# Kernel optimization log

Measured on AMD Instinct MI355X. Metric: run time of the kernel, lower is better.

The kernel has to match this reference:

```python
import jax, jax.numpy as jnp
import numpy as np

N, E, B = 50000, 800000, 128
H, L, FIN, GF = 256, 4, 8, 85
LN_EPS = 1e-5


def _ln(x, g, b):
    m = jnp.mean(x, axis=-1, keepdims=True)
    v = jnp.var(x, axis=-1, keepdims=True)
    return g * (x - m) * jax.lax.rsqrt(v + LN_EPS) + b


def setup_inputs() -> dict:
    key = jax.random.key(0)
    ks = iter(jax.random.split(key, 40))

    def nrm(shape, scale):
        return jax.random.normal(next(ks), shape, jnp.float32) * scale

    inp = {}
    inp["x"] = nrm((N, FIN), 1.0)
    inp["edge_index"] = jax.random.randint(next(ks), (2, E), 0, N, dtype=jnp.int32)
    inp["edge_weight"] = jax.random.uniform(next(ks), (E,), jnp.float32)
    inp["batch"] = jnp.sort(jax.random.randint(next(ks), (N,), 0, B, dtype=jnp.int32))
    inp["gene_feat"] = nrm((B, GF), 1.0)
    # input projection
    inp["W_in"] = nrm((FIN, H), FIN ** -0.5); inp["b_in"] = jnp.zeros((H,), jnp.float32)
    inp["ln_in_g"] = jnp.ones((H,), jnp.float32); inp["ln_in_b"] = jnp.zeros((H,), jnp.float32)
    # GIN layers (stacked over L)
    inp["eps"] = jnp.zeros((L,), jnp.float32)
    inp["W1"] = nrm((L, H, 2 * H), H ** -0.5); inp["b1"] = jnp.zeros((L, 2 * H), jnp.float32)
    inp["W2"] = nrm((L, 2 * H, H), (2 * H) ** -0.5); inp["b2"] = jnp.zeros((L, H), jnp.float32)
    inp["ln_g"] = jnp.ones((L, H), jnp.float32); inp["ln_b"] = jnp.zeros((L, H), jnp.float32)
    # gene feature projection
    inp["Wg1"] = nrm((GF, H), GF ** -0.5); inp["bg1"] = jnp.zeros((H,), jnp.float32)
    inp["lng_g"] = jnp.ones((H,), jnp.float32); inp["lng_b"] = jnp.zeros((H,), jnp.float32)
    inp["Wg2"] = nrm((H, H // 2), H ** -0.5); inp["bg2"] = jnp.zeros((H // 2,), jnp.float32)
    # classifier (embed_dim = 2H + H//2 = 640)
    ED = 2 * H + H // 2
    inp["Wc1"] = nrm((ED, H), ED ** -0.5); inp["bc1"] = jnp.zeros((H,), jnp.float32)
    inp["Wc2"] = nrm((H, H // 2), H ** -0.5); inp["bc2"] = jnp.zeros((H // 2,), jnp.float32)
    inp["Wc3"] = nrm((H // 2, 2), (H // 2) ** -0.5); inp["bc3"] = jnp.zeros((2,), jnp.float32)
    return inp


def reference(x, edge_index, edge_weight, batch, gene_feat,
              W_in, b_in, ln_in_g, ln_in_b,
              eps, W1, b1, W2, b2, ln_g, ln_b,
              Wg1, bg1, lng_g, lng_b, Wg2, bg2,
              Wc1, bc1, Wc2, bc2, Wc3, bc3):
    n = x.shape[0]
    nb = gene_feat.shape[0]
    # input projection: Linear -> LayerNorm -> ReLU  (dropout = eval mode)
    h = jax.nn.relu(_ln(x @ W_in + b_in, ln_in_g, ln_in_b))
    src, dst = edge_index[0], edge_index[1]
    for i in range(W1.shape[0]):
        res = h
        # weighted GIN aggregation; self-loops with weight 1 fold into (2+eps)*h
        msg = h[src] * edge_weight[:, None]            # [E, H]
        agg = jax.ops.segment_sum(msg, dst, num_segments=n)
        out = (2.0 + eps[i]) * h + agg
        out = jax.nn.relu(out @ W1[i] + b1[i]) @ W2[i] + b2[i]
        h = jax.nn.relu(_ln(out, ln_g[i], ln_b[i])) + res
    # dual pooling (mean + max) per graph
    counts = jax.ops.segment_sum(jnp.ones((n,), h.dtype), batch, num_segments=nb)
    gmean = jax.ops.segment_sum(h, batch, num_segments=nb) / jnp.clip(counts, 1.0)[:, None]
    gmax = jax.ops.segment_max(h, batch, num_segments=nb)
    gmax = jnp.where(jnp.isfinite(gmax), gmax, 0.0)
    # gene feature projection
    gp = jax.nn.relu(_ln(gene_feat @ Wg1 + bg1, lng_g, lng_b))
    gp = jax.nn.relu(gp @ Wg2 + bg2)
    g = jnp.concatenate([gmean, gmax, gp], axis=-1)   # [B, 640]
    # classifier
    hc = jax.nn.relu(g @ Wc1 + bc1)
    hc = jax.nn.relu(hc @ Wc2 + bc2)
    return hc @ Wc3 + bc3
```

## Files before the change

### kernel.cpp

```cpp
#include <hip/hip_runtime.h>
#include <hip/hip_bf16.h>

#define N_NODES 50000
#define MP 50048
#define N_EDGES 800000
#define N_B 128
#define H_DIM 256
#define H2_DIM 512
#define FIN_DIM 8
#define GF_DIM 85
#define LN_EPS 1e-5f
#define SCAN_NBLK 196

typedef unsigned short u16;
typedef unsigned int u32;
typedef _Float16 f16;
typedef __attribute__((ext_vector_type(8))) _Float16 f16x8;
typedef __attribute__((ext_vector_type(8))) unsigned short u16x8;
typedef __attribute__((ext_vector_type(4))) float f32x4;

__device__ inline float relu_f(float x) { return x > 0.f ? x : 0.f; }

__device__ inline float h2f(u16 b) { f16 h; __builtin_memcpy(&h, &b, 2); return (float)h; }
__device__ inline u16 f2h(float x) { f16 h = (f16)x; u16 b; __builtin_memcpy(&b, &h, 2); return b; }

#define GLOAD16(gp, lp) __builtin_amdgcn_global_load_lds( \
    (const __attribute__((address_space(1))) void*)(gp),  \
    (__attribute__((address_space(3))) void*)(lp), 16, 0, 0)

__device__ inline void ln_stats_256(float v, float* sbuf, float& mean, float& rstd) {
    float s = v, s2 = v * v;
#pragma unroll
    for (int off = 32; off > 0; off >>= 1) {
        s += __shfl_down(s, off);
        s2 += __shfl_down(s2, off);
    }
    int t = threadIdx.x;
    if ((t & 63) == 0) { sbuf[t >> 6] = s; sbuf[4 + (t >> 6)] = s2; }
    __syncthreads();
    float ts = sbuf[0] + sbuf[1] + sbuf[2] + sbuf[3];
    float ts2 = sbuf[4] + sbuf[5] + sbuf[6] + sbuf[7];
    mean = ts * (1.f / H_DIM);
    float var = ts2 * (1.f / H_DIM) - mean * mean;
    rstd = rsqrtf(var + LN_EPS);
}

__global__ void k_input_proj(const float* __restrict__ x, const float* __restrict__ Wi,
                             const float* __restrict__ bi, const float* __restrict__ g,
                             const float* __restrict__ bb,
                             u16* __restrict__ Hh, u16* __restrict__ Hl) {
    int n = blockIdx.x, t = threadIdx.x;
    __shared__ float xs[FIN_DIM];
    __shared__ float sbuf[8];
    if (t < FIN_DIM) xs[t] = x[n * FIN_DIM + t];
    __syncthreads();
    float acc = bi[t];
#pragma unroll
    for (int k = 0; k < FIN_DIM; ++k) acc = fmaf(xs[k], Wi[k * H_DIM + t], acc);
    float mean, rstd;
    ln_stats_256(acc, sbuf, mean, rstd);
    float v = relu_f(g[t] * (acc - mean) * rstd + bb[t]);
    u16 hh = f2h(v);
    size_t o = (size_t)n * H_DIM + t;
    Hh[o] = hh;
    Hl[o] = f2h(v - h2f(hh));
}

__global__ void k_hist(const int* __restrict__ ei, int* __restrict__ deg) {
    int e = blockIdx.x * 256 + threadIdx.x;
    atomicAdd(&deg[ei[N_EDGES + e]], 1);
}

__global__ void k_scan1(const int* __restrict__ deg, int* __restrict__ row_start,
                        int* __restrict__ bsum) {
    __shared__ int s[256];
    int t = threadIdx.x, i = blockIdx.x * 256 + t;
    int v = (i < N_NODES) ? deg[i] : 0;
    s[t] = v;
    __syncthreads();
    for (int off = 1; off < 256; off <<= 1) {
        int x = (t >= off) ? s[t - off] : 0;
        __syncthreads();
        s[t] += x;
        __syncthreads();
    }
    if (i < N_NODES) row_start[i] = s[t] - v;
    if (t == 255) bsum[blockIdx.x] = s[255];
}

__global__ void k_scan2(int* __restrict__ bsum) {
    __shared__ int s[256];
    int t = threadIdx.x;
    int v = (t < SCAN_NBLK) ? bsum[t] : 0;
    s[t] = v;
    __syncthreads();
    for (int off = 1; off < 256; off <<= 1) {
        int x = (t >= off) ? s[t - off] : 0;
        __syncthreads();
        s[t] += x;
        __syncthreads();
    }
    if (t < SCAN_NBLK) bsum[t] = s[t] - v;
}

__global__ void k_scan3(int* __restrict__ row_start, const int* __restrict__ bsum) {
    int t = threadIdx.x, i = blockIdx.x * 256 + t;
    if (i < N_NODES) row_start[i] += bsum[blockIdx.x];
    if (i == 0) row_start[N_NODES] = N_EDGES;
}

__global__ void k_scatter(const int* __restrict__ ei, const float* __restrict__ ew,
                          const int* __restrict__ row_start, int* __restrict__ cursor,
                          int* __restrict__ csr_src, float* __restrict__ csr_w) {
    int e = blockIdx.x * 256 + threadIdx.x;
    int d = ei[N_EDGES + e];
    int p = atomicAdd(&cursor[d], 1);
    int i = row_start[d] + p;
    csr_src[i] = ei[e];
    csr_w[i] = ew[e];
}

__global__ void k_gbounds(const int* __restrict__ batch, int* __restrict__ gstart,
                          int* __restrict__ gcnt) {
    __shared__ int s[N_B + 1];
    int b = threadIdx.x;
    int lo = 0, hi = N_NODES;
    while (lo < hi) {
        int mid = (lo + hi) >> 1;
        if (batch[mid] < b) lo = mid + 1; else hi = mid;
    }
    s[b] = lo;
    if (b == 0) s[N_B] = N_NODES;
    __syncthreads();
    gstart[b] = s[b];
    gcnt[b] = s[b + 1] - s[b];
}

__global__ void k_agg(const u16* __restrict__ Hh, const u16* __restrict__ Hl,
                      const int* __restrict__ row_start,
                      const int* __restrict__ csr_src, const float* __restrict__ csr_w,
                      const float* __restrict__ eps, int layer,
                      u16* __restrict__ Ah) {
    const int n = blockIdx.x, t = threadIdx.x, wv = t >> 6, lane = t & 63;
    const int half = lane >> 5, sl = lane & 31;
    __shared__ int s_src[256];
    __shared__ float s_w[256];
    __shared__ float part[4][256];
    int start = row_start[n], end = row_start[n + 1];
    float a[8];
#pragma unroll
    for (int q = 0; q < 8; ++q) a[q] = 0.f;
    for (int e0 = start; e0 < end; e0 += 256) {
        int ne = end - e0; if (ne > 256) ne = 256;
        if (t < ne) { s_src[t] = csr_src[e0 + t]; s_w[t] = csr_w[e0 + t]; }
        __syncthreads();
        for (int j = wv * 2 + half; j < ne; j += 8) {
            int src = s_src[j];
            float w = s_w[j];
            u16x8 v = *reinterpret_cast<const u16x8*>(&Hh[(size_t)src * H_DIM + sl * 8]);
#pragma unroll
            for (int q = 0; q < 8; ++q) a[q] = fmaf(w, h2f(v[q]), a[q]);
        }
        __syncthreads();
    }
#pragma unroll
    for (int q = 0; q < 8; ++q) a[q] += __shfl_xor(a[q], 32);
    if (half == 0) {
        *reinterpret_cast<float4*>(&part[wv][sl * 8]) = (float4){a[0], a[1], a[2], a[3]};
        *reinterpret_cast<float4*>(&part[wv][sl * 8 + 4]) = (float4){a[4], a[5], a[6], a[7]};
    }
    __syncthreads();
    float sum = part[0][t] + part[1][t] + part[2][t] + part[3][t];
    size_t so = (size_t)n * H_DIM + t;
    float e2 = 2.0f + eps[layer];
    float hs = h2f(Hh[so]) + h2f(Hl[so]);
    Ah[so] = f2h(e2 * hs + sum);
}

__global__ void k_wprep(const float* __restrict__ W, u16* __restrict__ T, int R, int C) {
    __shared__ float tile[64][65];
    int c0 = blockIdx.x * 64, r0 = blockIdx.y * 64;
    const float* Wl = W + (size_t)blockIdx.z * R * C;
    u16* Tl_ = T + (size_t)blockIdx.z * R * C;
    int t = threadIdx.x;
    int col = t & 63, qr = t >> 6;
#pragma unroll
    for (int i = 0; i < 16; ++i) {
        int row = i * 4 + qr;
        tile[row][col] = Wl[(size_t)(r0 + row) * C + c0 + col];
    }
    __syncthreads();
#pragma unroll
    for (int i = 0; i < 16; ++i) {
        int crow = i * 4 + qr;
        Tl_[(size_t)(c0 + crow) * R + r0 + col] = f2h(tile[col][crow]);
    }
}

__global__ __launch_bounds__(256, 2) void k_mgemm1(
    const u16* __restrict__ Ah, const u16* __restrict__ Wt,
    const float* __restrict__ bias, u16* __restrict__ Ch) {
    __shared__ __align__(16) u16 sA[128 * 32];
    __shared__ __align__(16) u16 sB[128 * 32];
    const int t = threadIdx.x;
    const int wv = t >> 6, lane = t & 63;
    const int fr = lane & 15, kg = lane >> 4;
    const int m0 = blockIdx.x * 128, n0 = blockIdx.y * 128;
    const int wm = (wv >> 1) * 64, wn = (wv & 1) * 64;

    f32x4 acc[4][4];
#pragma unroll
    for (int i = 0; i < 4; ++i)
#pragma unroll
        for (int j = 0; j < 4; ++j) acc[i][j] = (f32x4){0.f, 0.f, 0.f, 0.f};

    for (int k0 = 0; k0 < 256; k0 += 32) {
#pragma unroll
        for (int is = 0; is < 2; ++is) {
            int chunk = wv * 128 + is * 64 + lane;
            int r = chunk >> 2, p = chunk & 3;
            int ps = p ^ ((r >> 1) & 3);
            size_t ea = (size_t)(m0 + r) * 256 + k0 + ps * 8;
            size_t eb = (size_t)(n0 + r) * 256 + k0 + ps * 8;
            int lbase = (wv * 128 + is * 64) * 8;
            GLOAD16(Ah + ea, &sA[lbase]);
            GLOAD16(Wt + eb, &sB[lbase]);
        }
        __syncthreads();
        f16x8 fa[4], fb[4];
#pragma unroll
        for (int mf = 0; mf < 4; ++mf) {
            int row = wm + mf * 16 + fr;
            fa[mf] = *(const f16x8*)&sA[row * 32 + ((kg ^ ((row >> 1) & 3)) << 3)];
        }
#pragma unroll
        for (int nf = 0; nf < 4; ++nf) {
            int row = wn + nf * 16 + fr;
            fb[nf] = *(const f16x8*)&sB[row * 32 + ((kg ^ ((row >> 1) & 3)) << 3)];
        }
#pragma unroll
        for (int mf = 0; mf < 4; ++mf)
#pragma unroll
            for (int nf = 0; nf < 4; ++nf)
                acc[mf][nf] = __builtin_amdgcn_mfma_f32_16x16x32_f16(fa[mf], fb[nf], acc[mf][nf], 0, 0, 0);
        __syncthreads();
    }
#pragma unroll
    for (int nf = 0; nf < 4; ++nf) {
        int col = n0 + wn + nf * 16 + fr;
        float bi = bias[col];
#pragma unroll
        for (int mf = 0; mf < 4; ++mf)
#pragma unroll
            for (int j = 0; j < 4; ++j) {
                int grow = m0 + wm + mf * 16 + kg * 4 + j;
                Ch[(size_t)grow * 512 + col] = f2h(relu_f(acc[mf][nf][j] + bi));
            }
    }
}

__global__ __launch_bounds__(256, 2) void k_mgemm2(
    const u16* __restrict__ Ah, const u16* __restrict__ Wt,
    const float* __restrict__ bias, const float* __restrict__ lg,
    const float* __restrict__ lbv,
    const u16* __restrict__ Rh, const u16* __restrict__ Rl,
    u16* __restrict__ Oh, u16* __restrict__ Ol) {
    __shared__ __align__(16) u16 sA[64 * 32];
    __shared__ __align__(16) u16 sB[256 * 32];
    __shared__ float lnS[64][4], lnS2[64][4];
    __shared__ float lnm[64], lnr[64];
    const int t = threadIdx.x;
    const int wv = t >> 6, lane = t & 63;
    const int fr = lane & 15, kg = lane >> 4;
    const int m0 = blockIdx.x * 64;

    f32x4 acc[4][4];
#pragma unroll
    for (int i = 0; i < 4; ++i)
#pragma unroll
        for (int j = 0; j < 4; ++j) acc[i][j] = (f32x4){0.f, 0.f, 0.f, 0.f};

    for (int k0 = 0; k0 < 512; k0 += 32) {
        {
            int r = t >> 2, p = t & 3;
            int ps = p ^ ((r >> 1) & 3);
            size_t ea = (size_t)(m0 + r) * 512 + k0 + ps * 8;
            int lbase = (wv * 64) * 8;
            GLOAD16(Ah + ea, &sA[lbase]);
        }
#pragma unroll
        for (int is = 0; is < 4; ++is) {
            int chunk = is * 256 + t;
            int r = chunk >> 2, p = chunk & 3;
            int ps = p ^ ((r >> 1) & 3);
            size_t eb = (size_t)r * 512 + k0 + ps * 8;
            int lbase = (is * 256 + wv * 64) * 8;
            GLOAD16(Wt + eb, &sB[lbase]);
        }
        __syncthreads();
        f16x8 fa[4], fb[4];
#pragma unroll
        for (int mf = 0; mf < 4; ++mf) {
            int row = mf * 16 + fr;
            fa[mf] = *(const f16x8*)&sA[row * 32 + ((kg ^ ((row >> 1) & 3)) << 3)];
        }
#pragma unroll
        for (int nf = 0; nf < 4; ++nf) {
            int row = wv * 64 + nf * 16 + fr;
            fb[nf] = *(const f16x8*)&sB[row * 32 + ((kg ^ ((row >> 1) & 3)) << 3)];
        }
#pragma unroll
        for (int mf = 0; mf < 4; ++mf)
#pragma unroll
            for (int nf = 0; nf < 4; ++nf)
                acc[mf][nf] = __builtin_amdgcn_mfma_f32_16x16x32_f16(fa[mf], fb[nf], acc[mf][nf], 0, 0, 0);
        __syncthreads();
    }
    float bcol[4];
#pragma unroll
    for (int nf = 0; nf < 4; ++nf) bcol[nf] = bias[wv * 64 + nf * 16 + fr];
#pragma unroll
    for (int mf = 0; mf < 4; ++mf)
#pragma unroll
        for (int nf = 0; nf < 4; ++nf)
#pragma unroll
            for (int j = 0; j < 4; ++j) acc[mf][nf][j] += bcol[nf];
#pragma unroll
    for (int mf = 0; mf < 4; ++mf)
#pragma unroll
        for (int j = 0; j < 4; ++j) {
            float s = acc[mf][0][j] + acc[mf][1][j] + acc[mf][2][j] + acc[mf][3][j];
            float s2 = acc[mf][0][j] * acc[mf][0][j] + acc[mf][1][j] * acc[mf][1][j] +
                       acc[mf][2][j] * acc[mf][2][j] + acc[mf][3][j] * acc[mf][3][j];
#pragma unroll
            for (int off = 1; off < 16; off <<= 1) {
                s += __shfl_xor(s, off);
                s2 += __shfl_xor(s2, off);
            }
            if (fr == 0) {
                int row = mf * 16 + kg * 4 + j;
                lnS[row][wv] = s;
                lnS2[row][wv] = s2;
            }
        }
    __syncthreads();
    if (t < 64) {
        float s = lnS[t][0] + lnS[t][1] + lnS[t][2] + lnS[t][3];
        float s2 = lnS2[t][0] + lnS2[t][1] + lnS2[t][2] + lnS2[t][3];
        float m = s * (1.f / 256.f);
        float var = s2 * (1.f / 256.f) - m * m;
        lnm[t] = m;
        lnr[t] = rsqrtf(var + LN_EPS);
    }
    __syncthreads();
    float gg[4], bb[4];
#pragma unroll
    for (int nf = 0; nf < 4; ++nf) {
        int col = wv * 64 + nf * 16 + fr;
        gg[nf] = lg[col];
        bb[nf] = lbv[col];
    }
#pragma unroll
    for (int mf = 0; mf < 4; ++mf)
#pragma unroll
        for (int j = 0; j < 4; ++j) {
            int row = mf * 16 + kg * 4 + j;
            int grow = m0 + row;
            float m = lnm[row], rs = lnr[row];
#pragma unroll
            for (int nf = 0; nf < 4; ++nf) {
                int col = wv * 64 + nf * 16 + fr;
                size_t o = (size_t)grow * 256 + col;
                float res = h2f(Rh[o]) + h2f(Rl[o]);
                float v = relu_f(gg[nf] * (acc[mf][nf][j] - m) * rs + bb[nf]) + res;
                u16 hh = f2h(v);
                Oh[o] = hh;
                Ol[o] = f2h(v - h2f(hh));
            }
        }
}

__global__ void k_pool(const u16* __restrict__ Hh, const u16* __restrict__ Hl,
                       const int* __restrict__ gstart,
                       const int* __restrict__ gcnt, float* __restrict__ g) {
    int b = blockIdx.x;
    int col = blockIdx.y * 64 + (threadIdx.x & 63);
    int r = threadIdx.x >> 6;
    int st = gstart[b], cnt = gcnt[b];
    float s = 0.f, mx = -3.4e38f;
    for (int i = r; i < cnt; i += 4) {
        size_t o = (size_t)(st + i) * H_DIM + col;
        float v = h2f(Hh[o]) + h2f(Hl[o]);
        s += v;
        mx = fmaxf(mx, v);
    }
    __shared__ float ss[256], sm[256];
    ss[threadIdx.x] = s;
    sm[threadIdx.x] = mx;
    __syncthreads();
    if (r == 0) {
#pragma unroll
        for (int k = 1; k < 4; ++k) {
            s += ss[threadIdx.x + 64 * k];
            mx = fmaxf(mx, sm[threadIdx.x + 64 * k]);
        }
        float mean = cnt > 0 ? s / (float)cnt : 0.f;
        if (cnt == 0) mx = 0.f;
        g[b * 640 + col] = mean;
        g[b * 640 + 256 + col] = mx;
    }
}

__global__ void k_gene(const float* __restrict__ gf, const float* __restrict__ Wg1,
                       const float* __restrict__ bg1, const float* __restrict__ lg,
                       const float* __restrict__ lb, const float* __restrict__ Wg2,
                       const float* __restrict__ bg2, float* __restrict__ g) {
    int b = blockIdx.x, t = threadIdx.x;
    __shared__ float xs[GF_DIM];
    __shared__ float sbuf[8];
    __shared__ float s1[H_DIM];
    if (t < GF_DIM) xs[t] = gf[b * GF_DIM + t];
    __syncthreads();
    float acc = bg1[t];
    for (int k = 0; k < GF_DIM; ++k) acc = fmaf(xs[k], Wg1[k * H_DIM + t], acc);
    float mean, rstd;
    ln_stats_256(acc, sbuf, mean, rstd);
    s1[t] = relu_f(lg[t] * (acc - mean) * rstd + lb[t]);
    __syncthreads();
    if (t < 128) {
        float a2 = bg2[t];
        for (int k = 0; k < H_DIM; ++k) a2 = fmaf(s1[k], Wg2[k * 128 + t], a2);
        g[b * 640 + 512 + t] = relu_f(a2);
    }
}

__global__ void k_cls(const float* __restrict__ g, const float* __restrict__ Wc1,
                      const float* __restrict__ bc1, const float* __restrict__ Wc2,
                      const float* __restrict__ bc2, const float* __restrict__ Wc3,
                      const float* __restrict__ bc3, float* __restrict__ out) {
    int b = blockIdx.x, t = threadIdx.x;
    __shared__ float gg[640];
    __shared__ float s1[256];
    __shared__ float s2[128];
    gg[t] = g[b * 640 + t];
    gg[t + 256] = g[b * 640 + 256 + t];
    if (t < 128) gg[t + 512] = g[b * 640 + 512 + t];
    __syncthreads();
    float a = bc1[t];
    for (int k = 0; k < 640; ++k) a = fmaf(gg[k], Wc1[k * 256 + t], a);
    s1[t] = relu_f(a);
    __syncthreads();
    if (t < 128) {
        float a2 = bc2[t];
        for (int k = 0; k < 256; ++k) a2 = fmaf(s1[k], Wc2[k * 128 + t], a2);
        s2[t] = relu_f(a2);
    }
    __syncthreads();
    if (t < 2) {
        float a3 = bc3[t];
        for (int k = 0; k < 128; ++k) a3 = fmaf(s2[k], Wc3[k * 2 + t], a3);
        out[b * 2 + t] = a3;
    }
}

extern "C" void kernel_launch(void* const* d_in, const int* in_sizes, int n_in,
                              void* d_out, int out_size, void* d_ws, size_t ws_size,
                              hipStream_t stream) {
    const float* x = (const float*)d_in[0];
    const int* ei = (const int*)d_in[1];
    const float* ew = (const float*)d_in[2];
    const int* batch = (const int*)d_in[3];
    const float* gf = (const float*)d_in[4];
    const float* W_in = (const float*)d_in[5];
    const float* b_in = (const float*)d_in[6];
    const float* ln_in_g = (const float*)d_in[7];
    const float* ln_in_b = (const float*)d_in[8];
    const float* eps = (const float*)d_in[9];
    const float* W1 = (const float*)d_in[10];
    const float* b1 = (const float*)d_in[11];
    const float* W2 = (const float*)d_in[12];
    const float* b2 = (const float*)d_in[13];
    const float* ln_g = (const float*)d_in[14];
    const float* ln_b = (const float*)d_in[15];
    const float* Wg1 = (const float*)d_in[16];
    const float* bg1 = (const float*)d_in[17];
    const float* lng_g = (const float*)d_in[18];
    const float* lng_b = (const float*)d_in[19];
    const float* Wg2 = (const float*)d_in[20];
    const float* bg2 = (const float*)d_in[21];
    const float* Wc1 = (const float*)d_in[22];
    const float* bc1 = (const float*)d_in[23];
    const float* Wc2 = (const float*)d_in[24];
    const float* bc2 = (const float*)d_in[25];
    const float* Wc3 = (const float*)d_in[26];
    const float* bc3 = (const float*)d_in[27];
    float* out = (float*)d_out;

    char* ws = (char*)d_ws;
    size_t off = 0;
    auto alloc = [&](size_t bytes) -> char* {
        char* p = ws + off;
        off += (bytes + 255) & ~(size_t)255;
        return p;
    };
    u16* Hh0 = (u16*)alloc((size_t)MP * H_DIM * 2);
    u16* Hl0 = (u16*)alloc((size_t)MP * H_DIM * 2);
    u16* Hh1 = (u16*)alloc((size_t)MP * H_DIM * 2);
    u16* Hl1 = (u16*)alloc((size_t)MP * H_DIM * 2);
    u16* Ah = (u16*)alloc((size_t)MP * H_DIM * 2);
    u16* C1h = (u16*)alloc((size_t)MP * H2_DIM * 2);
    u16* W1T = (u16*)alloc((size_t)4 * H2_DIM * H_DIM * 2);
    u16* W2T = (u16*)alloc((size_t)4 * H_DIM * H2_DIM * 2);
    int* deg = (int*)alloc(N_NODES * 4);
    int* cursor = (int*)alloc(N_NODES * 4);
    int* row_start = (int*)alloc((N_NODES + 1) * 4);
    int* bsum = (int*)alloc(256 * 4);
    int* gcnt = (int*)alloc(N_B * 4);
    int* gstart = (int*)alloc(N_B * 4);
    int* csr_src = (int*)alloc(N_EDGES * 4);
    float* csr_w = (float*)alloc(N_EDGES * 4);
    float* gbuf = (float*)alloc(N_B * 640 * 4);
    (void)ws_size; (void)in_sizes; (void)n_in; (void)out_size;

    hipMemsetAsync(deg, 0, (size_t)((char*)row_start - (char*)deg), stream);

    k_wprep<<<dim3(H2_DIM / 64, H_DIM / 64, 4), 256, 0, stream>>>(W1, W1T, H_DIM, H2_DIM);
    k_wprep<<<dim3(H_DIM / 64, H2_DIM / 64, 4), 256, 0, stream>>>(W2, W2T, H2_DIM, H_DIM);

    k_input_proj<<<N_NODES, 256, 0, stream>>>(x, W_in, b_in, ln_in_g, ln_in_b, Hh0, Hl0);
    k_hist<<<N_EDGES / 256, 256, 0, stream>>>(ei, deg);
    k_scan1<<<SCAN_NBLK, 256, 0, stream>>>(deg, row_start, bsum);
    k_scan2<<<1, 256, 0, stream>>>(bsum);
    k_scan3<<<SCAN_NBLK, 256, 0, stream>>>(row_start, bsum);
    k_scatter<<<N_EDGES / 256, 256, 0, stream>>>(ei, ew, row_start, cursor, csr_src, csr_w);
    k_gbounds<<<1, N_B, 0, stream>>>(batch, gstart, gcnt);

    u16* hch = Hh0; u16* hcl = Hl0;
    u16* hnh = Hh1; u16* hnl = Hl1;
    for (int l = 0; l < 4; ++l) {
        k_agg<<<N_NODES, 256, 0, stream>>>(hch, hcl, row_start, csr_src, csr_w, eps, l, Ah);
        k_mgemm1<<<dim3(MP / 128, 4), 256, 0, stream>>>(
            Ah, W1T + (size_t)l * H2_DIM * H_DIM,
            b1 + (size_t)l * H2_DIM, C1h);
        k_mgemm2<<<MP / 64, 256, 0, stream>>>(
            C1h, W2T + (size_t)l * H_DIM * H2_DIM,
            b2 + (size_t)l * H_DIM, ln_g + (size_t)l * H_DIM, ln_b + (size_t)l * H_DIM,
            hch, hcl, hnh, hnl);
        u16* th = hch; hch = hnh; hnh = th;
        u16* tl = hcl; hcl = hnl; hnl = tl;
    }

    k_pool<<<dim3(N_B, 4), 256, 0, stream>>>(hch, hcl, gstart, gcnt, gbuf);
    k_gene<<<N_B, 256, 0, stream>>>(gf, Wg1, bg1, lng_g, lng_b, Wg2, bg2, gbuf);
    k_cls<<<N_B, 256, 0, stream>>>(gbuf, Wc1, bc1, Wc2, bc2, Wc3, bc3, out);
}
```

Before: 815.8 us.

## Use one 32-lane group per node in aggregation and widen GEMM K-tiles

The aggregation kernel now gives each node to a 32-lane group, with eight nodes per block, instead of one 256-thread block per node. Neighbor loads are unrolled by four, and the shared-memory staging, barriers and cross-wave reduction are removed. Both MFMA GEMMs now stage K tiles of 64 instead of 32 with a wider XOR swizzle, halving the number of barrier-separated K iterations. This trades more LDS per block and more registers, which could lower occupancy, for fewer syncs and more memory-level parallelism in the gather.

```diff
diff --git a/kernel.cpp b/kernel.cpp
--- a/kernel.cpp
+++ b/kernel.cpp
@@ -141,40 +141,45 @@
                       const int* __restrict__ csr_src, const float* __restrict__ csr_w,
                       const float* __restrict__ eps, int layer,
                       u16* __restrict__ Ah) {
-    const int n = blockIdx.x, t = threadIdx.x, wv = t >> 6, lane = t & 63;
-    const int half = lane >> 5, sl = lane & 31;
-    __shared__ int s_src[256];
-    __shared__ float s_w[256];
-    __shared__ float part[4][256];
+    const int t = threadIdx.x;
+    const int n = blockIdx.x * 8 + (t >> 5);
+    const int sl = t & 31;
     int start = row_start[n], end = row_start[n + 1];
     float a[8];
 #pragma unroll
     for (int q = 0; q < 8; ++q) a[q] = 0.f;
-    for (int e0 = start; e0 < end; e0 += 256) {
-        int ne = end - e0; if (ne > 256) ne = 256;
-        if (t < ne) { s_src[t] = csr_src[e0 + t]; s_w[t] = csr_w[e0 + t]; }
-        __syncthreads();
-        for (int j = wv * 2 + half; j < ne; j += 8) {
-            int src = s_src[j];
-            float w = s_w[j];
-            u16x8 v = *reinterpret_cast<const u16x8*>(&Hh[(size_t)src * H_DIM + sl * 8]);
-#pragma unroll
-            for (int q = 0; q < 8; ++q) a[q] = fmaf(w, h2f(v[q]), a[q]);
-        }
-        __syncthreads();
-    }
-#pragma unroll
-    for (int q = 0; q < 8; ++q) a[q] += __shfl_xor(a[q], 32);
-    if (half == 0) {
-        *reinterpret_cast<float4*>(&part[wv][sl * 8]) = (float4){a[0], a[1], a[2], a[3]};
-        *reinterpret_cast<float4*>(&part[wv][sl * 8 + 4]) = (float4){a[4], a[5], a[6], a[7]};
-    }
-    __syncthreads();
-    float sum = part[0][t] + part[1][t] + part[2][t] + part[3][t];
-    size_t so = (size_t)n * H_DIM + t;
+    int e = start;
+    for (; e + 3 < end; e += 4) {
+        int s0 = csr_src[e], s1 = csr_src[e + 1], s2 = csr_src[e + 2], s3 = csr_src[e + 3];
+        float w0 = csr_w[e], w1 = csr_w[e + 1], w2 = csr_w[e + 2], w3 = csr_w[e + 3];
+        u16x8 v0 = *reinterpret_cast<const u16x8*>(&Hh[(size_t)s0 * H_DIM + sl * 8]);
+        u16x8 v1 = *reinterpret_cast<const u16x8*>(&Hh[(size_t)s1 * H_DIM + sl * 8]);
+        u16x8 v2 = *reinterpret_cast<const u16x8*>(&Hh[(size_t)s2 * H_DIM + sl * 8]);
+        u16x8 v3 = *reinterpret_cast<const u16x8*>(&Hh[(size_t)s3 * H_DIM + sl * 8]);
+#pragma unroll
+        for (int q = 0; q < 8; ++q) {
+            a[q] = fmaf(w0, h2f(v0[q]), a[q]);
+            a[q] = fmaf(w1, h2f(v1[q]), a[q]);
+            a[q] = fmaf(w2, h2f(v2[q]), a[q]);
+            a[q] = fmaf(w3, h2f(v3[q]), a[q]);
+        }
+    }
+    for (; e < end; ++e) {
+        int src = csr_src[e];
+        float w = csr_w[e];
+        u16x8 v = *reinterpret_cast<const u16x8*>(&Hh[(size_t)src * H_DIM + sl * 8]);
+#pragma unroll
+        for (int q = 0; q < 8; ++q) a[q] = fmaf(w, h2f(v[q]), a[q]);
+    }
+    size_t so = (size_t)n * H_DIM + sl * 8;
     float e2 = 2.0f + eps[layer];
-    float hs = h2f(Hh[so]) + h2f(Hl[so]);
-    Ah[so] = f2h(e2 * hs + sum);
+    u16x8 hh = *reinterpret_cast<const u16x8*>(&Hh[so]);
+    u16x8 hl = *reinterpret_cast<const u16x8*>(&Hl[so]);
+    u16x8 o;
+#pragma unroll
+    for (int q = 0; q < 8; ++q)
+        o[q] = f2h(e2 * (h2f(hh[q]) + h2f(hl[q])) + a[q]);
+    *reinterpret_cast<u16x8*>(&Ah[so]) = o;
 }
 
 __global__ void k_wprep(const float* __restrict__ W, u16* __restrict__ T, int R, int C) {
@@ -200,8 +205,8 @@
 __global__ __launch_bounds__(256, 2) void k_mgemm1(
     const u16* __restrict__ Ah, const u16* __restrict__ Wt,
     const float* __restrict__ bias, u16* __restrict__ Ch) {
-    __shared__ __align__(16) u16 sA[128 * 32];
-    __shared__ __align__(16) u16 sB[128 * 32];
+    __shared__ __align__(16) u16 sA[128 * 64];
+    __shared__ __align__(16) u16 sB[128 * 64];
     const int t = threadIdx.x;
     const int wv = t >> 6, lane = t & 63;
     const int fr = lane & 15, kg = lane >> 4;
@@ -214,35 +219,43 @@
 #pragma unroll
         for (int j = 0; j < 4; ++j) acc[i][j] = (f32x4){0.f, 0.f, 0.f, 0.f};
 
-    for (int k0 = 0; k0 < 256; k0 += 32) {
-#pragma unroll
-        for (int is = 0; is < 2; ++is) {
-            int chunk = wv * 128 + is * 64 + lane;
-            int r = chunk >> 2, p = chunk & 3;
-            int ps = p ^ ((r >> 1) & 3);
-            size_t ea = (size_t)(m0 + r) * 256 + k0 + ps * 8;
-            size_t eb = (size_t)(n0 + r) * 256 + k0 + ps * 8;
-            int lbase = (wv * 128 + is * 64) * 8;
-            GLOAD16(Ah + ea, &sA[lbase]);
-            GLOAD16(Wt + eb, &sB[lbase]);
-        }
-        __syncthreads();
-        f16x8 fa[4], fb[4];
+    for (int k0 = 0; k0 < 256; k0 += 64) {
+#pragma unroll
+        for (int i = 0; i < 4; ++i) {
+            int ch = i * 256 + t;
+            int r = ch >> 3, p = ch & 7;
+            int ps = p ^ (r & 7);
+            int lbase = (i * 256 + wv * 64) * 8;
+            GLOAD16(Ah + (size_t)(m0 + r) * 256 + k0 + ps * 8, &sA[lbase]);
+            GLOAD16(Wt + (size_t)(n0 + r) * 256 + k0 + ps * 8, &sB[lbase]);
+        }
+        __syncthreads();
+        f16x8 fa[4][2], fb[4][2];
 #pragma unroll
         for (int mf = 0; mf < 4; ++mf) {
             int row = wm + mf * 16 + fr;
-            fa[mf] = *(const f16x8*)&sA[row * 32 + ((kg ^ ((row >> 1) & 3)) << 3)];
+#pragma unroll
+            for (int kk = 0; kk < 2; ++kk) {
+                int qs = (kk * 4 + kg) ^ (row & 7);
+                fa[mf][kk] = *(const f16x8*)&sA[row * 64 + qs * 8];
+            }
         }
 #pragma unroll
         for (int nf = 0; nf < 4; ++nf) {
             int row = wn + nf * 16 + fr;
-            fb[nf] = *(const f16x8*)&sB[row * 32 + ((kg ^ ((row >> 1) & 3)) << 3)];
-        }
-#pragma unroll
-        for (int mf = 0; mf < 4; ++mf)
-#pragma unroll
-            for (int nf = 0; nf < 4; ++nf)
-                acc[mf][nf] = __builtin_amdgcn_mfma_f32_16x16x32_f16(fa[mf], fb[nf], acc[mf][nf], 0, 0, 0);
+#pragma unroll
+            for (int kk = 0; kk < 2; ++kk) {
+                int qs = (kk * 4 + kg) ^ (row & 7);
+                fb[nf][kk] = *(const f16x8*)&sB[row * 64 + qs * 8];
+            }
+        }
+#pragma unroll
+        for (int kk = 0; kk < 2; ++kk)
+#pragma unroll
+            for (int mf = 0; mf < 4; ++mf)
+#pragma unroll
+                for (int nf = 0; nf < 4; ++nf)
+                    acc[mf][nf] = __builtin_amdgcn_mfma_f32_16x16x32_f16(fa[mf][kk], fb[nf][kk], acc[mf][nf], 0, 0, 0);
         __syncthreads();
     }
 #pragma unroll
@@ -265,8 +278,8 @@
     const float* __restrict__ lbv,
     const u16* __restrict__ Rh, const u16* __restrict__ Rl,
     u16* __restrict__ Oh, u16* __restrict__ Ol) {
-    __shared__ __align__(16) u16 sA[64 * 32];
-    __shared__ __align__(16) u16 sB[256 * 32];
+    __shared__ __align__(16) u16 sA[64 * 64];
+    __shared__ __align__(16) u16 sB[256 * 64];
     __shared__ float lnS[64][4], lnS2[64][4];
     __shared__ float lnm[64], lnr[64];
     const int t = threadIdx.x;
@@ -280,40 +293,48 @@
 #pragma unroll
         for (int j = 0; j < 4; ++j) acc[i][j] = (f32x4){0.f, 0.f, 0.f, 0.f};
 
-    for (int k0 = 0; k0 < 512; k0 += 32) {
-        {
-            int r = t >> 2, p = t & 3;
-            int ps = p ^ ((r >> 1) & 3);
-            size_t ea = (size_t)(m0 + r) * 512 + k0 + ps * 8;
-            int lbase = (wv * 64) * 8;
-            GLOAD16(Ah + ea, &sA[lbase]);
-        }
-#pragma unroll
-        for (int is = 0; is < 4; ++is) {
-            int chunk = is * 256 + t;
-            int r = chunk >> 2, p = chunk & 3;
-            int ps = p ^ ((r >> 1) & 3);
-            size_t eb = (size_t)r * 512 + k0 + ps * 8;
-            int lbase = (is * 256 + wv * 64) * 8;
-            GLOAD16(Wt + eb, &sB[lbase]);
-        }
-        __syncthreads();
-        f16x8 fa[4], fb[4];
+    for (int k0 = 0; k0 < 512; k0 += 64) {
+#pragma unroll
+        for (int i = 0; i < 2; ++i) {
+            int ch = i * 256 + t;
+            int r = ch >> 3, p = ch & 7;
+            int ps = p ^ (r & 7);
+            GLOAD16(Ah + (size_t)(m0 + r) * 512 + k0 + ps * 8, &sA[(i * 256 + wv * 64) * 8]);
+        }
+#pragma unroll
+        for (int i = 0; i < 8; ++i) {
+            int ch = i * 256 + t;
+            int r = ch >> 3, p = ch & 7;
+            int ps = p ^ (r & 7);
+            GLOAD16(Wt + (size_t)r * 512 + k0 + ps * 8, &sB[(i * 256 + wv * 64) * 8]);
+        }
+        __syncthreads();
+        f16x8 fa[4][2], fb[4][2];
 #pragma unroll
         for (int mf = 0; mf < 4; ++mf) {
             int row = mf * 16 + fr;
-            fa[mf] = *(const f16x8*)&sA[row * 32 + ((kg ^ ((row >> 1) & 3)) << 3)];
+#pragma unroll
+            for (int kk = 0; kk < 2; ++kk) {
+                int qs = (kk * 4 + kg) ^ (row & 7);
+                fa[mf][kk] = *(const f16x8*)&sA[row * 64 + qs * 8];
+            }
         }
 #pragma unroll
         for (int nf = 0; nf < 4; ++nf) {
             int row = wv * 64 + nf * 16 + fr;
-            fb[nf] = *(const f16x8*)&sB[row * 32 + ((kg ^ ((row >> 1) & 3)) << 3)];
-        }
-#pragma unroll
-        for (int mf = 0; mf < 4; ++mf)
-#pragma unroll
-            for (int nf = 0; nf < 4; ++nf)
-                acc[mf][nf] = __builtin_amdgcn_mfma_f32_16x16x32_f16(fa[mf], fb[nf], acc[mf][nf], 0, 0, 0);
+#pragma unroll
+            for (int kk = 0; kk < 2; ++kk) {
+                int qs = (kk * 4 + kg) ^ (row & 7);
+                fb[nf][kk] = *(const f16x8*)&sB[row * 64 + qs * 8];
+            }
+        }
+#pragma unroll
+        for (int kk = 0; kk < 2; ++kk)
+#pragma unroll
+            for (int mf = 0; mf < 4; ++mf)
+#pragma unroll
+                for (int nf = 0; nf < 4; ++nf)
+                    acc[mf][nf] = __builtin_amdgcn_mfma_f32_16x16x32_f16(fa[mf][kk], fb[nf][kk], acc[mf][nf], 0, 0, 0);
         __syncthreads();
     }
     float bcol[4];
@@ -538,7 +559,7 @@
     u16* hch = Hh0; u16* hcl = Hl0;
     u16* hnh = Hh1; u16* hnl = Hl1;
     for (int l = 0; l < 4; ++l) {
-        k_agg<<<N_NODES, 256, 0, stream>>>(hch, hcl, row_start, csr_src, csr_w, eps, l, Ah);
+        k_agg<<<N_NODES / 8, 256, 0, stream>>>(hch, hcl, row_start, csr_src, csr_w, eps, l, Ah);
         k_mgemm1<<<dim3(MP / 128, 4), 256, 0, stream>>>(
             Ah, W1T + (size_t)l * H2_DIM * H_DIM,
             b1 + (size_t)l * H2_DIM, C1h);
```

After: 761.2 us. -6.7%, faster.
